# Kernel tuning notes

Measured on AMD Instinct MI355X. Metric: run time of the kernel, lower is better.

## Reference

```python
import jax, jax.numpy as jnp
import numpy as np

B, T, S = 2, 1024, 1024
D, H, L = 512, 8, 4
E, K, FF = 8, 2, 2048
V, BLK = 32000, 2048
DH = D // H
EPS = 1e-5


def setup_inputs() -> dict:
    key = jax.random.key(0)
    ks = jax.random.split(key, 20)
    n = lambda k, shp: jax.random.normal(k, shp, dtype=jnp.float32) * 0.02
    return {
        "decoder_input_ids": jax.random.randint(ks[0], (B, T), 0, V, dtype=jnp.int32),
        "enc_out": jax.random.normal(ks[1], (B, S, D), dtype=jnp.float32),
        "attention_mask": jnp.ones((B, T), dtype=jnp.int32),
        "embed_table": n(ks[2], (V, D)),
        "pos_table": n(ks[3], (BLK, D)),
        "sa_w": n(ks[4], (L, 4, D, D)),   # q,k,v,o projections for self-attn
        "sa_b": jnp.zeros((L, 4, D), jnp.float32),
        "ca_w": n(ks[5], (L, 4, D, D)),   # q,k,v,o projections for cross-attn
        "ca_b": jnp.zeros((L, 4, D), jnp.float32),
        "ln_g": jnp.ones((L, 3, D), jnp.float32),
        "ln_b": jnp.zeros((L, 3, D), jnp.float32),
        "router_w": n(ks[6], (L, D, E)),
        "router_b": jnp.zeros((L, E), jnp.float32),
        "exp_w1": n(ks[7], (L, E, D, FF)),
        "exp_b1": jnp.zeros((L, E, FF), jnp.float32),
        "exp_w2": n(ks[8], (L, E, FF, D)),
        "exp_b2": jnp.zeros((L, E, D), jnp.float32),
    }


def _layer_norm(x, g, b):
    mu = jnp.mean(x, axis=-1, keepdims=True)
    var = jnp.mean(jnp.square(x - mu), axis=-1, keepdims=True)
    return (x - mu) * jax.lax.rsqrt(var + EPS) * g + b


def _mha(q_in, kv_in, w, b, mask):
    # w: [4, D, D]; 0=q,1=k,2=v,3=out
    def split_heads(t):
        Bn, Tn, _ = t.shape
        return t.reshape(Bn, Tn, H, DH).transpose(0, 2, 1, 3)  # [B,H,T,dh]
    q = split_heads(q_in @ w[0] + b[0])
    k = split_heads(kv_in @ w[1] + b[1])
    v = split_heads(kv_in @ w[2] + b[2])
    scores = jnp.einsum("bhqd,bhkd->bhqk", q, k) / jnp.sqrt(jnp.float32(DH))
    if mask is not None:
        scores = jnp.where(mask, scores, jnp.float32(-1e9))
    attn = jax.nn.softmax(scores, axis=-1)
    out = jnp.einsum("bhqk,bhkd->bhqd", attn, v)
    out = out.transpose(0, 2, 1, 3).reshape(q_in.shape[0], q_in.shape[1], D)
    return out @ w[3] + b[3]


def _sparse_moe(x, rw, rb, w1, b1, w2, b2):
    # Router: softmax over experts, keep top-k, renormalize kept weights.
    logits = x @ rw + rb                       # [B,T,E]
    probs = jax.nn.softmax(logits, axis=-1)
    topv, topi = jax.lax.top_k(probs, K)       # [B,T,K]
    kmask = jnp.sum(jax.nn.one_hot(topi, E, dtype=x.dtype), axis=-2)  # [B,T,E]
    gates = probs * kmask
    gates = gates / jnp.sum(gates, axis=-1, keepdims=True)
    # Dense expert compute (faithful math, vectorized over experts).
    h = jax.nn.relu(jnp.einsum("btd,edf->btef", x, w1) + b1)   # [B,T,E,FF]
    eo = jnp.einsum("btef,efd->bted", h, w2) + b2              # [B,T,E,D]
    out = jnp.einsum("bte,bted->btd", gates, eo)
    # Load-balancing aux loss: E * sum_e f_e * P_e
    f = jnp.mean(kmask, axis=(0, 1))
    p = jnp.mean(probs, axis=(0, 1))
    lb = jnp.float32(E) * jnp.sum(f * p)
    return out, lb


def reference(decoder_input_ids, enc_out, attention_mask, embed_table, pos_table,
              sa_w, sa_b, ca_w, ca_b, ln_g, ln_b, router_w, router_b,
              exp_w1, exp_b1, exp_w2, exp_b2):
    Bn, Tn = decoder_input_ids.shape
    y = embed_table[decoder_input_ids] + pos_table[:Tn]  # [B,T,D]
    causal = jnp.tril(jnp.ones((Tn, Tn), dtype=bool))
    am = attention_mask.astype(bool)[:, None, None, :]   # [B,1,1,T]
    mask = causal[None, None] & am                       # [B,1,T,T]
    lb_total = jnp.float32(0.0)
    for i in range(L):
        sa = _mha(y, y, sa_w[i], sa_b[i], mask)
        y = _layer_norm(y + sa, ln_g[i, 0], ln_b[i, 0])
        ca = _mha(y, enc_out, ca_w[i], ca_b[i], None)
        y = _layer_norm(y + ca, ln_g[i, 1], ln_b[i, 1])
        mo, lb = _sparse_moe(y, router_w[i], router_b[i], exp_w1[i], exp_b1[i], exp_w2[i], exp_b2[i])
        lb_total = lb_total + lb
        y = _layer_norm(y + mo, ln_g[i, 2], ln_b[i, 2])
    return y, lb_total
```

## Files before the change

kernel.cpp:

```cpp
#include <hip/hip_runtime.h>
#include <math.h>

#define Bb 2
#define Tt 1024
#define Ss 1024
#define Dd 512
#define Hh 8
#define Ll 4
#define Ee 8
#define FFf 2048
#define Mm 2048
#define NPp 4096
#define EPSF 1e-5f
#define DD_ (Dd*Dd)
#define LOSC 1024.0f
#define ILOSC (1.0f/1024.0f)
#define RBLK 64
#define IMm (1.0f/(float)Mm)

typedef _Float16 f16;
typedef __attribute__((ext_vector_type(8))) _Float16 f16x8;
typedef __attribute__((ext_vector_type(4))) _Float16 f16x4;
typedef __attribute__((ext_vector_type(4))) float f32x4;

__device__ __forceinline__ void fsplit(float x, f16& h, f16& l) {
  h = (f16)x;
  l = (f16)((x - (float)h) * LOSC);
}

__device__ __forceinline__ void load16(const void* g, void* l) {
  __builtin_amdgcn_global_load_lds(
      (const __attribute__((address_space(1))) void*)g,
      (__attribute__((address_space(3))) void*)l, 16, 0, 0);
}

__global__ void embed_kernel(const int* __restrict__ ids,
                             const float* __restrict__ emb,
                             const float* __restrict__ pos,
                             float* __restrict__ Y,
                             f16* __restrict__ Yh, f16* __restrict__ Yl) {
  int m = blockIdx.x;
  int t = m % Tt;
  int id = ids[m];
  for (int d = threadIdx.x; d < Dd; d += 256) {
    float v = emb[(size_t)id * Dd + d] + pos[(size_t)t * Dd + d];
    Y[(size_t)m * Dd + d] = v;
    f16 h, l; fsplit(v, h, l);
    Yh[(size_t)m * Dd + d] = h;
    Yl[(size_t)m * Dd + d] = l;
  }
}

__global__ void cvt_split_kernel(const float* __restrict__ src,
                                 f16* __restrict__ dh, f16* __restrict__ dl) {
  size_t i = ((size_t)blockIdx.x * 256 + threadIdx.x) * 4;
  float4 v = *reinterpret_cast<const float4*>(&src[i]);
  float a[4] = {v.x, v.y, v.z, v.w};
#pragma unroll
  for (int j = 0; j < 4; j++) { f16 h, l; fsplit(a[j], h, l); dh[i + j] = h; dl[i + j] = l; }
}

__global__ __launch_bounds__(256)
void transpose_split(const float* __restrict__ src,
                     f16* __restrict__ dstH, f16* __restrict__ dstL,
                     int Kd, int Nd) {
  __shared__ float Tl[32][33];
  size_t zo = (size_t)blockIdx.z * Kd * Nd;
  int k0 = blockIdx.y * 32, n0 = blockIdx.x * 32;
  int t = threadIdx.x;
  int r = t >> 3, c = t & 7;
  float4 v = *reinterpret_cast<const float4*>(&src[zo + (size_t)(k0 + r) * Nd + n0 + c * 4]);
  Tl[r][c * 4 + 0] = v.x; Tl[r][c * 4 + 1] = v.y;
  Tl[r][c * 4 + 2] = v.z; Tl[r][c * 4 + 3] = v.w;
  __syncthreads();
  int nl = t >> 3, kq = t & 7;
  f16x4 hv, lv;
#pragma unroll
  for (int i = 0; i < 4; i++) {
    f16 h, l; fsplit(Tl[kq * 4 + i][nl], h, l);
    hv[i] = h; lv[i] = l;
  }
  size_t o = zo + (size_t)(n0 + nl) * Kd + k0 + kq * 4;
  *reinterpret_cast<f16x4*>(&dstH[o]) = hv;
  *reinterpret_cast<f16x4*>(&dstL[o]) = lv;
}

template <bool GATHER, bool OSPLIT, bool RELU, bool GATE, int KS>
__global__ __launch_bounds__(256)
void mm128(const f16* __restrict__ Ah_, const f16* __restrict__ Al_, int lda,
           const f16* __restrict__ Bh_, const f16* __restrict__ Bl_,
           const float* __restrict__ bias,
           float* __restrict__ Cf, f16* __restrict__ Ch, f16* __restrict__ Cl, int ldc,
           int Mtot, int N, int K,
           const int* __restrict__ tok, const float* __restrict__ gate,
           const int* __restrict__ offs, const int* __restrict__ cnt) {
  __shared__ f16 Ash[2][128 * 32];
  __shared__ f16 Asl[2][128 * 32];
  __shared__ f16 Bsh[2][128 * 32];
  __shared__ f16 Bsl[2][128 * 32];
  int zz = blockIdx.z;
  int e  = (KS > 1) ? (zz / KS) : zz;
  int ks = (KS > 1) ? (zz % KS) : 0;
  int base = 0, ne = Mtot;
  if (offs) { base = offs[e]; ne = cnt[e]; }
  int m0 = blockIdx.y * 128;
  if (m0 >= ne) return;
  int rem = ne - m0;
  Bh_ += (size_t)e * N * K;
  Bl_ += (size_t)e * N * K;
  bias += (size_t)e * N;
  if (KS > 1) Cf += (size_t)ks * (size_t)Mtot * (size_t)ldc;

  int t = threadIdx.x;
  int rr = t >> 2, cc = t & 3;
  int csw = cc ^ ((rr >> 1) & 3);
  int gr0 = base + m0 + rr;      if (gr0 > Mtot - 1) gr0 = Mtot - 1;
  int gr1 = base + m0 + rr + 64; if (gr1 > Mtot - 1) gr1 = Mtot - 1;
  int arow0 = GATHER ? tok[gr0] : gr0;
  int arow1 = GATHER ? tok[gr1] : gr1;
  size_t aoff0 = (size_t)arow0 * lda + csw * 8;
  size_t aoff1 = (size_t)arow1 * lda + csw * 8;
  size_t boff0 = (size_t)(blockIdx.x * 128 + rr) * K + csw * 8;
  size_t boff1 = (size_t)(blockIdx.x * 128 + rr + 64) * K + csw * 8;

  int lane = t & 63, wv = t >> 6;
  int quad = lane >> 4, m16 = lane & 15;
  int sw = quad ^ ((m16 >> 1) & 3);
  int wm = (wv >> 1) * 64, wn = (wv & 1) * 64;

  f32x4 accm[4][4], accc[4][4];
#pragma unroll
  for (int i = 0; i < 4; i++)
#pragma unroll
    for (int j = 0; j < 4; j++) {
      accm[i][j] = (f32x4){0.f, 0.f, 0.f, 0.f};
      accc[i][j] = (f32x4){0.f, 0.f, 0.f, 0.f};
    }

  int kper = K / KS;
  int kbeg = ks * kper;
  int nt = kper >> 5;

  auto STAGE = [&](int bf, int kc) {
    load16(Ah_ + aoff0 + kc, &Ash[bf][t * 8]);
    load16(Ah_ + aoff1 + kc, &Ash[bf][2048 + t * 8]);
    load16(Al_ + aoff0 + kc, &Asl[bf][t * 8]);
    load16(Al_ + aoff1 + kc, &Asl[bf][2048 + t * 8]);
    load16(Bh_ + boff0 + kc, &Bsh[bf][t * 8]);
    load16(Bh_ + boff1 + kc, &Bsh[bf][2048 + t * 8]);
    load16(Bl_ + boff0 + kc, &Bsl[bf][t * 8]);
    load16(Bl_ + boff1 + kc, &Bsl[bf][2048 + t * 8]);
  };

  STAGE(0, kbeg);
  asm volatile("s_waitcnt vmcnt(0)" ::: "memory");
  __builtin_amdgcn_s_barrier();

  for (int tt = 0; tt < nt; ++tt) {
    int bf = tt & 1;
    if (tt + 1 < nt) STAGE(bf ^ 1, kbeg + (tt + 1) * 32);
    f16x8 ah[4], al[4];
#pragma unroll
    for (int i = 0; i < 4; i++) {
      ah[i] = *reinterpret_cast<const f16x8*>(&Ash[bf][(wm + i * 16 + m16) * 32 + sw * 8]);
      al[i] = *reinterpret_cast<const f16x8*>(&Asl[bf][(wm + i * 16 + m16) * 32 + sw * 8]);
    }
#pragma unroll
    for (int j = 0; j < 4; j++) {
      f16x8 bh = *reinterpret_cast<const f16x8*>(&Bsh[bf][(wn + j * 16 + m16) * 32 + sw * 8]);
      f16x8 bl = *reinterpret_cast<const f16x8*>(&Bsl[bf][(wn + j * 16 + m16) * 32 + sw * 8]);
#pragma unroll
      for (int i = 0; i < 4; i++) {
        accm[i][j] = __builtin_amdgcn_mfma_f32_16x16x32_f16(ah[i], bh, accm[i][j], 0, 0, 0);
        accc[i][j] = __builtin_amdgcn_mfma_f32_16x16x32_f16(ah[i], bl, accc[i][j], 0, 0, 0);
        accc[i][j] = __builtin_amdgcn_mfma_f32_16x16x32_f16(al[i], bh, accc[i][j], 0, 0, 0);
      }
    }
    asm volatile("s_waitcnt vmcnt(0)" ::: "memory");
    __builtin_amdgcn_s_barrier();
  }

#pragma unroll
  for (int i = 0; i < 4; i++) {
#pragma unroll
    for (int reg = 0; reg < 4; reg++) {
      int lr = wm + i * 16 + quad * 4 + reg;
      if (lr < rem) {
        size_t grow = (size_t)(base + m0 + lr);
        float gv = 1.f;
        if (GATE) gv = gate[grow];
#pragma unroll
        for (int j = 0; j < 4; j++) {
          int col = blockIdx.x * 128 + wn + j * 16 + m16;
          float bv = (KS == 1 || ks == 0) ? bias[col] : 0.f;
          float v = accm[i][j][reg] + accc[i][j][reg] * ILOSC + bv;
          if (RELU) v = fmaxf(v, 0.f);
          if (GATE) v *= gv;
          if (OSPLIT) {
            f16 h, l; fsplit(v, h, l);
            Ch[grow * ldc + col] = h;
            Cl[grow * ldc + col] = l;
          } else {
            Cf[grow * ldc + col] = v;
          }
        }
      }
    }
  }
}

__global__ __launch_bounds__(256)
void attn_mfma(const f16* __restrict__ Qh, const f16* __restrict__ Ql, int sq, int oq,
               const f16* __restrict__ Kh, const f16* __restrict__ Kl, int sk, int ok,
               const f16* __restrict__ Vh, const f16* __restrict__ Vl, int sv, int ov,
               f16* __restrict__ Oh, f16* __restrict__ Ol,
               const int* __restrict__ amask, int causal, int nK) {
  __shared__ f16 Ksh[32 * 64];
  __shared__ f16 Ksl[32 * 64];
  __shared__ f16 Vth[64 * 32];
  __shared__ f16 Vtl[64 * 32];
  __shared__ f16 Psh[4 * 16 * 32];
  __shared__ f16 Psl[4 * 16 * 32];

  int bh = blockIdx.x;
  int b = bh >> 3, hd = bh & 7;
  int t = threadIdx.x;
  int wv = t >> 6, lane = t & 63;
  int quad = lane >> 4, m16 = lane & 15;
  int qfrow = blockIdx.y * 64 + wv * 16 + m16;
  int qcbase = blockIdx.y * 64 + wv * 16 + quad * 4;

  size_t qoff = (size_t)(b * Tt + qfrow) * sq + oq + hd * 64;
  f16x8 qh0 = *reinterpret_cast<const f16x8*>(Qh + qoff + quad * 8);
  f16x8 qh1 = *reinterpret_cast<const f16x8*>(Qh + qoff + 32 + quad * 8);
  f16x8 ql0 = *reinterpret_cast<const f16x8*>(Ql + qoff + quad * 8);
  f16x8 ql1 = *reinterpret_cast<const f16x8*>(Ql + qoff + 32 + quad * 8);

  f32x4 Om[4], Oc[4];
#pragma unroll
  for (int c = 0; c < 4; c++) {
    Om[c] = (f32x4){0.f, 0.f, 0.f, 0.f};
    Oc[c] = (f32x4){0.f, 0.f, 0.f, 0.f};
  }
  float mr[4] = {-1e30f, -1e30f, -1e30f, -1e30f};
  float lrw[4] = {0.f, 0.f, 0.f, 0.f};

  int NT = causal ? (blockIdx.y * 2 + 2) : (nK >> 5);
  int myNT = causal ? (((blockIdx.y * 64 + wv * 16 + 15) >> 5) + 1) : NT;

  int rk = t >> 3, gs = t & 7, gsrc = gs ^ (rk & 7);
  int rv = t & 31, gv = t >> 5;

  for (int kt = 0; kt < NT; ++kt) {
    __syncthreads();
    {
      size_t krow = (size_t)(b * 1024 + kt * 32 + rk) * sk + ok + hd * 64 + gsrc * 8;
      *reinterpret_cast<f16x8*>(&Ksh[t * 8]) = *reinterpret_cast<const f16x8*>(Kh + krow);
      *reinterpret_cast<f16x8*>(&Ksl[t * 8]) = *reinterpret_cast<const f16x8*>(Kl + krow);
      size_t vrow = (size_t)(b * 1024 + kt * 32 + rv) * sv + ov + hd * 64 + gv * 8;
      f16x8 vh8 = *reinterpret_cast<const f16x8*>(Vh + vrow);
      f16x8 vl8 = *reinterpret_cast<const f16x8*>(Vl + vrow);
#pragma unroll
      for (int i = 0; i < 8; i++) {
        Vth[(gv * 8 + i) * 32 + rv] = vh8[i];
        Vtl[(gv * 8 + i) * 32 + rv] = vl8[i];
      }
    }
    __syncthreads();

    if (kt < myNT) {
      f32x4 S0m = (f32x4){0.f, 0.f, 0.f, 0.f}, S0c = S0m, S1m = S0m, S1c = S0m;
      {
        int key0 = m16, key1 = 16 + m16;
        int g0a = (quad) ^ (key0 & 7), g0b = (4 + quad) ^ (key0 & 7);
        int g1a = (quad) ^ (key1 & 7), g1b = (4 + quad) ^ (key1 & 7);
        f16x8 kh0a = *reinterpret_cast<const f16x8*>(&Ksh[key0 * 64 + g0a * 8]);
        f16x8 kh0b = *reinterpret_cast<const f16x8*>(&Ksh[key0 * 64 + g0b * 8]);
        f16x8 kl0a = *reinterpret_cast<const f16x8*>(&Ksl[key0 * 64 + g0a * 8]);
        f16x8 kl0b = *reinterpret_cast<const f16x8*>(&Ksl[key0 * 64 + g0b * 8]);
        S0m = __builtin_amdgcn_mfma_f32_16x16x32_f16(qh0, kh0a, S0m, 0, 0, 0);
        S0m = __builtin_amdgcn_mfma_f32_16x16x32_f16(qh1, kh0b, S0m, 0, 0, 0);
        S0c = __builtin_amdgcn_mfma_f32_16x16x32_f16(qh0, kl0a, S0c, 0, 0, 0);
        S0c = __builtin_amdgcn_mfma_f32_16x16x32_f16(qh1, kl0b, S0c, 0, 0, 0);
        S0c = __builtin_amdgcn_mfma_f32_16x16x32_f16(ql0, kh0a, S0c, 0, 0, 0);
        S0c = __builtin_amdgcn_mfma_f32_16x16x32_f16(ql1, kh0b, S0c, 0, 0, 0);
        f16x8 kh1a = *reinterpret_cast<const f16x8*>(&Ksh[key1 * 64 + g1a * 8]);
        f16x8 kh1b = *reinterpret_cast<const f16x8*>(&Ksh[key1 * 64 + g1b * 8]);
        f16x8 kl1a = *reinterpret_cast<const f16x8*>(&Ksl[key1 * 64 + g1a * 8]);
        f16x8 kl1b = *reinterpret_cast<const f16x8*>(&Ksl[key1 * 64 + g1b * 8]);
        S1m = __builtin_amdgcn_mfma_f32_16x16x32_f16(qh0, kh1a, S1m, 0, 0, 0);
        S1m = __builtin_amdgcn_mfma_f32_16x16x32_f16(qh1, kh1b, S1m, 0, 0, 0);
        S1c = __builtin_amdgcn_mfma_f32_16x16x32_f16(qh0, kl1a, S1c, 0, 0, 0);
        S1c = __builtin_amdgcn_mfma_f32_16x16x32_f16(qh1, kl1b, S1c, 0, 0, 0);
        S1c = __builtin_amdgcn_mfma_f32_16x16x32_f16(ql0, kh1a, S1c, 0, 0, 0);
        S1c = __builtin_amdgcn_mfma_f32_16x16x32_f16(ql1, kh1b, S1c, 0, 0, 0);
      }
      float S0[4], S1[4];
      int key0 = kt * 32 + m16, key1 = kt * 32 + 16 + m16;
      int am0 = amask ? amask[b * nK + key0] : 1;
      int am1 = amask ? amask[b * nK + key1] : 1;
#pragma unroll
      for (int reg = 0; reg < 4; reg++) {
        int qr = qcbase + reg;
        bool ok0 = am0 && (!causal || key0 <= qr);
        bool ok1 = am1 && (!causal || key1 <= qr);
        S0[reg] = ok0 ? (S0m[reg] + S0c[reg] * ILOSC) * 0.125f : -1e9f;
        S1[reg] = ok1 ? (S1m[reg] + S1c[reg] * ILOSC) * 0.125f : -1e9f;
      }
      float mt[4], al4[4], rs[4];
#pragma unroll
      for (int reg = 0; reg < 4; reg++) mt[reg] = fmaxf(S0[reg], S1[reg]);
#pragma unroll
      for (int off = 1; off < 16; off <<= 1)
#pragma unroll
        for (int reg = 0; reg < 4; reg++) mt[reg] = fmaxf(mt[reg], __shfl_xor(mt[reg], off, 64));
#pragma unroll
      for (int reg = 0; reg < 4; reg++) {
        float mn = fmaxf(mr[reg], mt[reg]);
        al4[reg] = expf(mr[reg] - mn);
        mr[reg] = mn;
        S0[reg] = expf(S0[reg] - mn);
        S1[reg] = expf(S1[reg] - mn);
        rs[reg] = S0[reg] + S1[reg];
      }
#pragma unroll
      for (int off = 1; off < 16; off <<= 1)
#pragma unroll
        for (int reg = 0; reg < 4; reg++) rs[reg] += __shfl_xor(rs[reg], off, 64);
#pragma unroll
      for (int reg = 0; reg < 4; reg++) {
        lrw[reg] = lrw[reg] * al4[reg] + rs[reg];
#pragma unroll
        for (int c = 0; c < 4; c++) { Om[c][reg] *= al4[reg]; Oc[c][reg] *= al4[reg]; }
        int prow = wv * 16 + quad * 4 + reg;
        f16 ph, pl;
        fsplit(S0[reg], ph, pl);
        Psh[prow * 32 + m16] = ph; Psl[prow * 32 + m16] = pl;
        fsplit(S1[reg], ph, pl);
        Psh[prow * 32 + 16 + m16] = ph; Psl[prow * 32 + 16 + m16] = pl;
      }
      __builtin_amdgcn_sched_barrier(0);
      f16x8 pah = *reinterpret_cast<const f16x8*>(&Psh[(wv * 16 + m16) * 32 + quad * 8]);
      f16x8 pal = *reinterpret_cast<const f16x8*>(&Psl[(wv * 16 + m16) * 32 + quad * 8]);
#pragma unroll
      for (int c = 0; c < 4; c++) {
        f16x8 vbh = *reinterpret_cast<const f16x8*>(&Vth[(c * 16 + m16) * 32 + quad * 8]);
        f16x8 vbl = *reinterpret_cast<const f16x8*>(&Vtl[(c * 16 + m16) * 32 + quad * 8]);
        Om[c] = __builtin_amdgcn_mfma_f32_16x16x32_f16(pah, vbh, Om[c], 0, 0, 0);
        Oc[c] = __builtin_amdgcn_mfma_f32_16x16x32_f16(pah, vbl, Oc[c], 0, 0, 0);
        Oc[c] = __builtin_amdgcn_mfma_f32_16x16x32_f16(pal, vbh, Oc[c], 0, 0, 0);
      }
    }
  }
#pragma unroll
  for (int reg = 0; reg < 4; reg++) {
    int qr = qcbase + reg;
    float inv = 1.f / lrw[reg];
#pragma unroll
    for (int c = 0; c < 4; c++) {
      float o = (Om[c][reg] + Oc[c][reg] * ILOSC) * inv;
      f16 hh, ll; fsplit(o, hh, ll);
      size_t oo = (size_t)(b * Tt + qr) * Dd + hd * 64 + c * 16 + m16;
      Oh[oo] = hh;
      Ol[oo] = ll;
    }
  }
}

__global__ __launch_bounds__(256)
void add_ln_kernel(float* __restrict__ Y, f16* __restrict__ Yh, f16* __restrict__ Yl,
                   const float* __restrict__ Aadd,
                   const float* __restrict__ g, const float* __restrict__ bb) {
  int tid = threadIdx.x;
  size_t base = (size_t)blockIdx.x * Dd;
  __shared__ float red[256];
  __shared__ float mu_s, rs_s;
  float x0 = Y[base + tid] + Aadd[base + tid];
  float x1 = Y[base + 256 + tid] + Aadd[base + 256 + tid];
  red[tid] = x0 + x1; __syncthreads();
  for (int s2 = 128; s2 > 0; s2 >>= 1) { if (tid < s2) red[tid] += red[tid + s2]; __syncthreads(); }
  if (tid == 0) mu_s = red[0] / (float)Dd;
  __syncthreads();
  float mu = mu_s;
  float d0 = x0 - mu, d1 = x1 - mu;
  red[tid] = d0 * d0 + d1 * d1; __syncthreads();
  for (int s2 = 128; s2 > 0; s2 >>= 1) { if (tid < s2) red[tid] += red[tid + s2]; __syncthreads(); }
  if (tid == 0) rs_s = rsqrtf(red[0] / (float)Dd + EPSF);
  __syncthreads();
  float rs = rs_s;
  float o0 = d0 * rs * g[tid] + bb[tid];
  float o1 = d1 * rs * g[256 + tid] + bb[256 + tid];
  f16 h, l;
  Y[base + tid] = o0; fsplit(o0, h, l); Yh[base + tid] = h; Yl[base + tid] = l;
  Y[base + 256 + tid] = o1; fsplit(o1, h, l); Yh[base + 256 + tid] = h; Yl[base + 256 + tid] = l;
}

__global__ __launch_bounds__(256)
void combine_ln_kernel(float* __restrict__ Y, f16* __restrict__ Yh, f16* __restrict__ Yl,
                       const float* __restrict__ pout, const float* __restrict__ pout2,
                       const int* __restrict__ slot,
                       const float* __restrict__ g, const float* __restrict__ bb) {
  int tid = threadIdx.x;
  int m = blockIdx.x;
  size_t base = (size_t)m * Dd;
  int s0 = slot[m * 2 + 0], s1 = slot[m * 2 + 1];
  __shared__ float red[256];
  __shared__ float mu_s, rs_s;
  float x0 = Y[base + tid] + pout[(size_t)s0 * Dd + tid] + pout[(size_t)s1 * Dd + tid]
           + pout2[(size_t)s0 * Dd + tid] + pout2[(size_t)s1 * Dd + tid];
  float x1 = Y[base + 256 + tid] + pout[(size_t)s0 * Dd + 256 + tid] + pout[(size_t)s1 * Dd + 256 + tid]
           + pout2[(size_t)s0 * Dd + 256 + tid] + pout2[(size_t)s1 * Dd + 256 + tid];
  red[tid] = x0 + x1; __syncthreads();
  for (int s2 = 128; s2 > 0; s2 >>= 1) { if (tid < s2) red[tid] += red[tid + s2]; __syncthreads(); }
  if (tid == 0) mu_s = red[0] / (float)Dd;
  __syncthreads();
  float mu = mu_s;
  float d0 = x0 - mu, d1 = x1 - mu;
  red[tid] = d0 * d0 + d1 * d1; __syncthreads();
  for (int s2 = 128; s2 > 0; s2 >>= 1) { if (tid < s2) red[tid] += red[tid + s2]; __syncthreads(); }
  if (tid == 0) rs_s = rsqrtf(red[0] / (float)Dd + EPSF);
  __syncthreads();
  float rs = rs_s;
  float o0 = d0 * rs * g[tid] + bb[tid];
  float o1 = d1 * rs * g[256 + tid] + bb[256 + tid];
  f16 h, l;
  Y[base + tid] = o0; fsplit(o0, h, l); Yh[base + tid] = h; Yl[base + tid] = l;
  Y[base + 256 + tid] = o1; fsplit(o1, h, l); Yh[base + 256 + tid] = h; Yl[base + 256 + tid] = l;
}

__global__ __launch_bounds__(256)
void router_kernel(const float* __restrict__ Y, const float* __restrict__ rw,
                   const float* __restrict__ rb, float* __restrict__ gates,
                   int* __restrict__ topi, int* __restrict__ part_cnt,
                   float* __restrict__ part_sumP) {
  int wv = threadIdx.x >> 6, lane = threadIdx.x & 63;
  __shared__ float wsum[4][Ee];
  __shared__ int wcnt[4][Ee];
  float w[8][Ee];
#pragma unroll
  for (int dd = 0; dd < 8; dd++) {
    const float4* rp = reinterpret_cast<const float4*>(&rw[(size_t)(dd * 64 + lane) * Ee]);
    float4 a = rp[0], b4 = rp[1];
    w[dd][0] = a.x; w[dd][1] = a.y; w[dd][2] = a.z; w[dd][3] = a.w;
    w[dd][4] = b4.x; w[dd][5] = b4.y; w[dd][6] = b4.z; w[dd][7] = b4.w;
  }
  float rbv[Ee];
#pragma unroll
  for (int e = 0; e < Ee; e++) rbv[e] = rb[e];

  float psum[Ee]; int pcnt[Ee];
#pragma unroll
  for (int e = 0; e < Ee; e++) { psum[e] = 0.f; pcnt[e] = 0; }

  int m0 = blockIdx.x * 32 + wv * 8;
  for (int j = 0; j < 8; j++) {
    int m = m0 + j;
    const float* yr = Y + (size_t)m * Dd;
    float yv[8];
#pragma unroll
    for (int dd = 0; dd < 8; dd++) yv[dd] = yr[dd * 64 + lane];
    float acc[Ee];
#pragma unroll
    for (int e = 0; e < Ee; e++) acc[e] = 0.f;
#pragma unroll
    for (int dd = 0; dd < 8; dd++)
#pragma unroll
      for (int e = 0; e < Ee; e++) acc[e] += yv[dd] * w[dd][e];
#pragma unroll
    for (int off = 32; off; off >>= 1)
#pragma unroll
      for (int e = 0; e < Ee; e++) acc[e] += __shfl_xor(acc[e], off, 64);
    if (lane == 0) {
      float pv[Ee];
      float mx = -1e30f;
#pragma unroll
      for (int e = 0; e < Ee; e++) { pv[e] = acc[e] + rbv[e]; mx = fmaxf(mx, pv[e]); }
      float ssum = 0.f;
#pragma unroll
      for (int e = 0; e < Ee; e++) { pv[e] = expf(pv[e] - mx); ssum += pv[e]; }
      float invs = 1.f / ssum;
#pragma unroll
      for (int e = 0; e < Ee; e++) { pv[e] *= invs; psum[e] += pv[e]; }
      int i1 = 0;
#pragma unroll
      for (int e = 1; e < Ee; e++) if (pv[e] > pv[i1]) i1 = e;
      int i2 = (i1 == 0) ? 1 : 0;
#pragma unroll
      for (int e = 0; e < Ee; e++) if (e != i1 && pv[e] > pv[i2]) i2 = e;
      float gs = pv[i1] + pv[i2];
      gates[m * 2 + 0] = pv[i1] / gs;
      gates[m * 2 + 1] = pv[i2] / gs;
      topi[m * 2 + 0] = i1;
      topi[m * 2 + 1] = i2;
#pragma unroll
      for (int e = 0; e < Ee; e++) pcnt[e] += (e == i1) + (e == i2);
    }
  }
  if (lane == 0) {
#pragma unroll
    for (int e = 0; e < Ee; e++) { wsum[wv][e] = psum[e]; wcnt[wv][e] = pcnt[e]; }
  }
  __syncthreads();
  if (threadIdx.x < Ee) {
    int e = threadIdx.x;
    float s = wsum[0][e] + wsum[1][e] + wsum[2][e] + wsum[3][e];
    int c = wcnt[0][e] + wcnt[1][e] + wcnt[2][e] + wcnt[3][e];
    part_sumP[blockIdx.x * Ee + e] = s;
    part_cnt[blockIdx.x * Ee + e] = c;
  }
}

__global__ void prefix_lb_kernel(const int* __restrict__ part_cnt,
                                 const float* __restrict__ part_sumP,
                                 int* __restrict__ cnt, int* __restrict__ offs,
                                 int* __restrict__ fill, float* __restrict__ lb_acc) {
  __shared__ int sc[Ee];
  __shared__ float ss[Ee];
  int t = threadIdx.x;
  if (t < Ee) {
    int c = 0; float s = 0.f;
    for (int b2 = 0; b2 < RBLK; b2++) { c += part_cnt[b2 * Ee + t]; s += part_sumP[b2 * Ee + t]; }
    sc[t] = c; ss[t] = s;
    cnt[t] = c; fill[t] = 0;
  }
  __syncthreads();
  if (t == 0) {
    int run = 0;
    float lb = 0.f;
    for (int e = 0; e < Ee; e++) {
      offs[e] = run; run += sc[e];
      lb += ((float)sc[e] * IMm) * (ss[e] * IMm);
    }
    *lb_acc += (float)Ee * lb;
  }
}

__global__ __launch_bounds__(256)
void scatter_kernel(const int* __restrict__ topi, const float* __restrict__ gates,
                    const int* __restrict__ offs, int* __restrict__ fill,
                    int* __restrict__ pair_tok, float* __restrict__ pair_gate,
                    int* __restrict__ slot) {
  __shared__ int lcnt[Ee];
  __shared__ int lbase[Ee];
  int t = threadIdx.x;
  int m = blockIdx.x * 256 + t;
  if (t < Ee) lcnt[t] = 0;
  __syncthreads();
  int e0 = topi[m * 2 + 0], e1 = topi[m * 2 + 1];
  float g0 = gates[m * 2 + 0], g1 = gates[m * 2 + 1];
  int p0 = atomicAdd(&lcnt[e0], 1);
  int p1 = atomicAdd(&lcnt[e1], 1);
  __syncthreads();
  if (t < Ee) lbase[t] = atomicAdd(&fill[t], lcnt[t]);
  __syncthreads();
  int i0 = offs[e0] + lbase[e0] + p0;
  int i1 = offs[e1] + lbase[e1] + p1;
  pair_tok[i0] = m; pair_gate[i0] = g0; slot[m * 2 + 0] = i0;
  pair_tok[i1] = m; pair_gate[i1] = g1; slot[m * 2 + 1] = i1;
}

__global__ void init_lb_kernel(float* lb_acc) {
  if (threadIdx.x == 0) *lb_acc = 0.f;
}

__global__ void finalize_kernel(const float* __restrict__ Y,
                                const float* __restrict__ lb_acc,
                                float* __restrict__ out) {
  size_t i = (size_t)blockIdx.x * 256 + threadIdx.x;
  const size_t n = (size_t)Mm * Dd;
  if (i < n) out[i] = Y[i];
  if (i == 0) out[n] = *lb_acc;
}

extern "C" void kernel_launch(void* const* d_in, const int* in_sizes, int n_in,
                              void* d_out, int out_size, void* d_ws, size_t ws_size,
                              hipStream_t stream) {
  const int*   ids   = (const int*)d_in[0];
  const float* enc   = (const float*)d_in[1];
  const int*   amask = (const int*)d_in[2];
  const float* emb   = (const float*)d_in[3];
  const float* pos   = (const float*)d_in[4];
  const float* sa_w  = (const float*)d_in[5];
  const float* sa_b  = (const float*)d_in[6];
  const float* ca_w  = (const float*)d_in[7];
  const float* ca_b  = (const float*)d_in[8];
  const float* ln_g  = (const float*)d_in[9];
  const float* ln_b  = (const float*)d_in[10];
  const float* rw    = (const float*)d_in[11];
  const float* rb    = (const float*)d_in[12];
  const float* ew1   = (const float*)d_in[13];
  const float* eb1   = (const float*)d_in[14];
  const float* ew2   = (const float*)d_in[15];
  const float* eb2   = (const float*)d_in[16];
  float* out = (float*)d_out;

  char* p = (char*)d_ws;
  auto alloc = [&](size_t bytes) { void* r = p; p += (bytes + 255) & ~(size_t)255; return r; };
  float* y    = (float*)alloc((size_t)Mm * Dd * 4);
  float* proj = (float*)alloc((size_t)Mm * Dd * 4);
  float* pout = (float*)alloc((size_t)2 * NPp * Dd * 4);
  f16* yh   = (f16*)alloc((size_t)Mm * Dd * 2);
  f16* yl   = (f16*)alloc((size_t)Mm * Dd * 2);
  f16* ench = (f16*)alloc((size_t)Mm * Dd * 2);
  f16* encl = (f16*)alloc((size_t)Mm * Dd * 2);
  f16* qkvh = (f16*)alloc((size_t)Mm * 1536 * 2);
  f16* qkvl = (f16*)alloc((size_t)Mm * 1536 * 2);
  f16* qch  = (f16*)alloc((size_t)Mm * Dd * 2);
  f16* qcl  = (f16*)alloc((size_t)Mm * Dd * 2);
  f16* atth = (f16*)alloc((size_t)Mm * Dd * 2);
  f16* attl = (f16*)alloc((size_t)Mm * Dd * 2);
  f16* ckvh = (f16*)alloc((size_t)Mm * 1024 * 2);
  f16* ckvl = (f16*)alloc((size_t)Mm * 1024 * 2);
  f16* moeh = (f16*)alloc((size_t)NPp * FFf * 2);
  f16* moel = (f16*)alloc((size_t)NPp * FFf * 2);
  f16* saTh = (f16*)alloc((size_t)Ll * 4 * DD_ * 2);
  f16* saTl = (f16*)alloc((size_t)Ll * 4 * DD_ * 2);
  f16* caTh = (f16*)alloc((size_t)Ll * 4 * DD_ * 2);
  f16* caTl = (f16*)alloc((size_t)Ll * 4 * DD_ * 2);
  f16* w1Th = (f16*)alloc((size_t)Ee * Dd * FFf * 2);
  f16* w1Tl = (f16*)alloc((size_t)Ee * Dd * FFf * 2);
  f16* w2Th = (f16*)alloc((size_t)Ee * Dd * FFf * 2);
  f16* w2Tl = (f16*)alloc((size_t)Ee * Dd * FFf * 2);
  float* gates     = (float*)alloc((size_t)Mm * 2 * 4);
  float* pair_gate = (float*)alloc((size_t)NPp * 4);
  float* part_sumP = (float*)alloc((size_t)RBLK * Ee * 4);
  float* lb_acc    = (float*)alloc(4);
  int* topi     = (int*)alloc((size_t)Mm * 2 * 4);
  int* pair_tok = (int*)alloc((size_t)NPp * 4);
  int* slot     = (int*)alloc((size_t)Mm * 2 * 4);
  int* part_cnt = (int*)alloc((size_t)RBLK * Ee * 4);
  int* cnt      = (int*)alloc(Ee * 4);
  int* offs     = (int*)alloc(Ee * 4);
  int* fill     = (int*)alloc(Ee * 4);
  float* pout2 = pout + (size_t)NPp * Dd;

  init_lb_kernel<<<1, 64, 0, stream>>>(lb_acc);
  embed_kernel<<<Mm, 256, 0, stream>>>(ids, emb, pos, y, yh, yl);
  cvt_split_kernel<<<(Mm * Dd) / 1024, 256, 0, stream>>>(enc, ench, encl);
  transpose_split<<<dim3(16, 16, 16), 256, 0, stream>>>(sa_w, saTh, saTl, Dd, Dd);
  transpose_split<<<dim3(16, 16, 16), 256, 0, stream>>>(ca_w, caTh, caTl, Dd, Dd);

  dim3 gAttn(Bb * Hh, Tt / 64);

  for (int i = 0; i < Ll; i++) {
    transpose_split<<<dim3(64, 16, 8), 256, 0, stream>>>(ew1 + (size_t)i * Ee * Dd * FFf, w1Th, w1Tl, Dd, FFf);
    transpose_split<<<dim3(16, 64, 8), 256, 0, stream>>>(ew2 + (size_t)i * Ee * FFf * Dd, w2Th, w2Tl, FFf, Dd);

    const f16* saThl = saTh + (size_t)i * 4 * DD_;
    const f16* saTll = saTl + (size_t)i * 4 * DD_;
    const f16* caThl = caTh + (size_t)i * 4 * DD_;
    const f16* caTll = caTl + (size_t)i * 4 * DD_;
    const float* sabl = sa_b + (size_t)i * 4 * Dd;
    const float* cabl = ca_b + (size_t)i * 4 * Dd;

    mm128<false, true, false, false, 1><<<dim3(8, 16, 1), 256, 0, stream>>>(
        ench, encl, Dd, caThl + DD_, caTll + DD_, cabl + Dd,
        nullptr, ckvh, ckvl, 1024, Mm, 1024, Dd, nullptr, nullptr, nullptr, nullptr);
    mm128<false, true, false, false, 1><<<dim3(12, 16, 1), 256, 0, stream>>>(
        yh, yl, Dd, saThl, saTll, sabl,
        nullptr, qkvh, qkvl, 1536, Mm, 1536, Dd, nullptr, nullptr, nullptr, nullptr);
    attn_mfma<<<gAttn, 256, 0, stream>>>(qkvh, qkvl, 1536, 0, qkvh, qkvl, 1536, 512,
                                         qkvh, qkvl, 1536, 1024, atth, attl, amask, 1, Tt);
    mm128<false, false, false, false, 1><<<dim3(4, 16, 1), 256, 0, stream>>>(
        atth, attl, Dd, saThl + 3 * DD_, saTll + 3 * DD_, sabl + 3 * Dd,
        proj, nullptr, nullptr, Dd, Mm, Dd, Dd, nullptr, nullptr, nullptr, nullptr);
    add_ln_kernel<<<Mm, 256, 0, stream>>>(y, yh, yl, proj,
                                          ln_g + (size_t)(i * 3 + 0) * Dd, ln_b + (size_t)(i * 3 + 0) * Dd);
    mm128<false, true, false, false, 1><<<dim3(4, 16, 1), 256, 0, stream>>>(
        yh, yl, Dd, caThl, caTll, cabl,
        nullptr, qch, qcl, Dd, Mm, Dd, Dd, nullptr, nullptr, nullptr, nullptr);
    attn_mfma<<<gAttn, 256, 0, stream>>>(qch, qcl, Dd, 0, ckvh, ckvl, 1024, 0,
                                         ckvh, ckvl, 1024, 512, atth, attl, nullptr, 0, Ss);
    mm128<false, false, false, false, 1><<<dim3(4, 16, 1), 256, 0, stream>>>(
        atth, attl, Dd, caThl + 3 * DD_, caTll + 3 * DD_, cabl + 3 * Dd,
        proj, nullptr, nullptr, Dd, Mm, Dd, Dd, nullptr, nullptr, nullptr, nullptr);
    add_ln_kernel<<<Mm, 256, 0, stream>>>(y, yh, yl, proj,
                                          ln_g + (size_t)(i * 3 + 1) * Dd, ln_b + (size_t)(i * 3 + 1) * Dd);
    router_kernel<<<RBLK, 256, 0, stream>>>(y, rw + (size_t)i * Dd * Ee, rb + (size_t)i * Ee,
                                            gates, topi, part_cnt, part_sumP);
    prefix_lb_kernel<<<1, 64, 0, stream>>>(part_cnt, part_sumP, cnt, offs, fill, lb_acc);
    scatter_kernel<<<Mm / 256, 256, 0, stream>>>(topi, gates, offs, fill, pair_tok, pair_gate, slot);
    mm128<true, true, true, false, 1><<<dim3(16, 32, 8), 256, 0, stream>>>(
        yh, yl, Dd, w1Th, w1Tl, eb1 + (size_t)i * Ee * FFf,
        nullptr, moeh, moel, FFf, NPp, FFf, Dd, pair_tok, nullptr, offs, cnt);
    mm128<false, false, false, true, 2><<<dim3(4, 32, Ee * 2), 256, 0, stream>>>(
        moeh, moel, FFf, w2Th, w2Tl, eb2 + (size_t)i * Ee * Dd,
        pout, nullptr, nullptr, Dd, NPp, Dd, FFf, nullptr, pair_gate, offs, cnt);
    combine_ln_kernel<<<Mm, 256, 0, stream>>>(y, yh, yl, pout, pout2, slot,
                                              ln_g + (size_t)(i * 3 + 2) * Dd, ln_b + (size_t)(i * 3 + 2) * Dd);
  }

  finalize_kernel<<<(int)(((size_t)Mm * Dd + 256) / 256) + 1, 256, 0, stream>>>(y, lb_acc, out);
}
```

Before: 2.437 ms.

## Pre-tile B weights, interleave MoE hidden hi/lo, and restructure GEMM pipeline waits

New measurement: 2.440 ms. No clear change (+0.1%).

```diff
diff --git a/kernel.cpp b/kernel.cpp
--- a/kernel.cpp
+++ b/kernel.cpp
@@ -80,12 +80,18 @@
     f16 h, l; fsplit(Tl[kq * 4 + i][nl], h, l);
     hv[i] = h; lv[i] = l;
   }
-  size_t o = zo + (size_t)(n0 + nl) * Kd + k0 + kq * 4;
+  int n = n0 + nl;
+  int nb = n >> 7, rr2 = n & 127;
+  int kb = k0 >> 5;
+  int s_orig = kq >> 1;
+  int s_pack = s_orig ^ ((rr2 >> 1) & 3);
+  size_t o = zo + (((size_t)nb * (size_t)(Kd >> 5) + kb) * 128 + rr2) * 32
+           + s_pack * 8 + (kq & 1) * 4;
   *reinterpret_cast<f16x4*>(&dstH[o]) = hv;
   *reinterpret_cast<f16x4*>(&dstL[o]) = lv;
 }
 
-template <bool GATHER, bool OSPLIT, bool RELU, bool GATE, int KS>
+template <bool GATHER, bool OSPLIT, bool RELU, bool GATE, int KS, bool AIL, bool CIL>
 __global__ __launch_bounds__(256)
 void mm128(const f16* __restrict__ Ah_, const f16* __restrict__ Al_, int lda,
            const f16* __restrict__ Bh_, const f16* __restrict__ Bl_,
@@ -118,10 +124,10 @@
   int gr1 = base + m0 + rr + 64; if (gr1 > Mtot - 1) gr1 = Mtot - 1;
   int arow0 = GATHER ? tok[gr0] : gr0;
   int arow1 = GATHER ? tok[gr1] : gr1;
-  size_t aoff0 = (size_t)arow0 * lda + csw * 8;
-  size_t aoff1 = (size_t)arow1 * lda + csw * 8;
-  size_t boff0 = (size_t)(blockIdx.x * 128 + rr) * K + csw * 8;
-  size_t boff1 = (size_t)(blockIdx.x * 128 + rr + 64) * K + csw * 8;
+  const size_t ldaa = (size_t)lda * (AIL ? 2 : 1);
+  size_t aoff0 = (size_t)arow0 * ldaa + csw * 8;
+  size_t aoff1 = (size_t)arow1 * ldaa + csw * 8;
+  size_t btile = (size_t)blockIdx.x * (size_t)(K >> 5) * 4096 + (size_t)t * 8;
 
   int lane = t & 63, wv = t >> 6;
   int quad = lane >> 4, m16 = lane & 15;
@@ -142,23 +148,30 @@
   int nt = kper >> 5;
 
   auto STAGE = [&](int bf, int kc) {
-    load16(Ah_ + aoff0 + kc, &Ash[bf][t * 8]);
-    load16(Ah_ + aoff1 + kc, &Ash[bf][2048 + t * 8]);
-    load16(Al_ + aoff0 + kc, &Asl[bf][t * 8]);
-    load16(Al_ + aoff1 + kc, &Asl[bf][2048 + t * 8]);
-    load16(Bh_ + boff0 + kc, &Bsh[bf][t * 8]);
-    load16(Bh_ + boff1 + kc, &Bsh[bf][2048 + t * 8]);
-    load16(Bl_ + boff0 + kc, &Bsl[bf][t * 8]);
-    load16(Bl_ + boff1 + kc, &Bsl[bf][2048 + t * 8]);
+    int kcA = AIL ? kc * 2 : kc;
+    load16(Ah_ + aoff0 + kcA, &Ash[bf][t * 8]);
+    load16(Ah_ + aoff1 + kcA, &Ash[bf][2048 + t * 8]);
+    load16(Al_ + aoff0 + kcA, &Asl[bf][t * 8]);
+    load16(Al_ + aoff1 + kcA, &Asl[bf][2048 + t * 8]);
+    size_t bb = btile + (size_t)(kc >> 5) * 4096;
+    load16(Bh_ + bb, &Bsh[bf][t * 8]);
+    load16(Bh_ + bb + 2048, &Bsh[bf][2048 + t * 8]);
+    load16(Bl_ + bb, &Bsl[bf][t * 8]);
+    load16(Bl_ + bb + 2048, &Bsl[bf][2048 + t * 8]);
   };
 
+  asm volatile("s_waitcnt vmcnt(0)" ::: "memory");
   STAGE(0, kbeg);
-  asm volatile("s_waitcnt vmcnt(0)" ::: "memory");
-  __builtin_amdgcn_s_barrier();
 
   for (int tt = 0; tt < nt; ++tt) {
     int bf = tt & 1;
-    if (tt + 1 < nt) STAGE(bf ^ 1, kbeg + (tt + 1) * 32);
+    if (tt + 1 < nt) {
+      STAGE(bf ^ 1, kbeg + (tt + 1) * 32);
+      asm volatile("s_waitcnt vmcnt(8)" ::: "memory");
+    } else {
+      asm volatile("s_waitcnt vmcnt(0)" ::: "memory");
+    }
+    __builtin_amdgcn_s_barrier();
     f16x8 ah[4], al[4];
 #pragma unroll
     for (int i = 0; i < 4; i++) {
@@ -176,7 +189,6 @@
         accc[i][j] = __builtin_amdgcn_mfma_f32_16x16x32_f16(al[i], bh, accc[i][j], 0, 0, 0);
       }
     }
-    asm volatile("s_waitcnt vmcnt(0)" ::: "memory");
     __builtin_amdgcn_s_barrier();
   }
 
@@ -198,8 +210,14 @@
           if (GATE) v *= gv;
           if (OSPLIT) {
             f16 h, l; fsplit(v, h, l);
-            Ch[grow * ldc + col] = h;
-            Cl[grow * ldc + col] = l;
+            if (CIL) {
+              size_t idx = grow * ((size_t)ldc * 2) + (size_t)((col >> 5) * 64 + (col & 31));
+              Ch[idx] = h;
+              Cl[idx] = l;
+            } else {
+              Ch[grow * ldc + col] = h;
+              Cl[grow * ldc + col] = l;
+            }
           } else {
             Cf[grow * ldc + col] = v;
           }
@@ -611,8 +629,7 @@
   f16* attl = (f16*)alloc((size_t)Mm * Dd * 2);
   f16* ckvh = (f16*)alloc((size_t)Mm * 1024 * 2);
   f16* ckvl = (f16*)alloc((size_t)Mm * 1024 * 2);
-  f16* moeh = (f16*)alloc((size_t)NPp * FFf * 2);
-  f16* moel = (f16*)alloc((size_t)NPp * FFf * 2);
+  f16* moe  = (f16*)alloc((size_t)NPp * FFf * 2 * 2);
   f16* saTh = (f16*)alloc((size_t)Ll * 4 * DD_ * 2);
   f16* saTl = (f16*)alloc((size_t)Ll * 4 * DD_ * 2);
   f16* caTh = (f16*)alloc((size_t)Ll * 4 * DD_ * 2);
@@ -653,25 +670,25 @@
     const float* sabl = sa_b + (size_t)i * 4 * Dd;
     const float* cabl = ca_b + (size_t)i * 4 * Dd;
 
-    mm128<false, true, false, false, 1><<<dim3(8, 16, 1), 256, 0, stream>>>(
+    mm128<false, true, false, false, 1, false, false><<<dim3(8, 16, 1), 256, 0, stream>>>(
         ench, encl, Dd, caThl + DD_, caTll + DD_, cabl + Dd,
         nullptr, ckvh, ckvl, 1024, Mm, 1024, Dd, nullptr, nullptr, nullptr, nullptr);
-    mm128<false, true, false, false, 1><<<dim3(12, 16, 1), 256, 0, stream>>>(
+    mm128<false, true, false, false, 1, false, false><<<dim3(12, 16, 1), 256, 0, stream>>>(
         yh, yl, Dd, saThl, saTll, sabl,
         nullptr, qkvh, qkvl, 1536, Mm, 1536, Dd, nullptr, nullptr, nullptr, nullptr);
     attn_mfma<<<gAttn, 256, 0, stream>>>(qkvh, qkvl, 1536, 0, qkvh, qkvl, 1536, 512,
                                          qkvh, qkvl, 1536, 1024, atth, attl, amask, 1, Tt);
-    mm128<false, false, false, false, 1><<<dim3(4, 16, 1), 256, 0, stream>>>(
+    mm128<false, false, false, false, 1, false, false><<<dim3(4, 16, 1), 256, 0, stream>>>(
         atth, attl, Dd, saThl + 3 * DD_, saTll + 3 * DD_, sabl + 3 * Dd,
         proj, nullptr, nullptr, Dd, Mm, Dd, Dd, nullptr, nullptr, nullptr, nullptr);
     add_ln_kernel<<<Mm, 256, 0, stream>>>(y, yh, yl, proj,
                                           ln_g + (size_t)(i * 3 + 0) * Dd, ln_b + (size_t)(i * 3 + 0) * Dd);
-    mm128<false, true, false, false, 1><<<dim3(4, 16, 1), 256, 0, stream>>>(
+    mm128<false, true, false, false, 1, false, false><<<dim3(4, 16, 1), 256, 0, stream>>>(
         yh, yl, Dd, caThl, caTll, cabl,
         nullptr, qch, qcl, Dd, Mm, Dd, Dd, nullptr, nullptr, nullptr, nullptr);
     attn_mfma<<<gAttn, 256, 0, stream>>>(qch, qcl, Dd, 0, ckvh, ckvl, 1024, 0,
                                          ckvh, ckvl, 1024, 512, atth, attl, nullptr, 0, Ss);
-    mm128<false, false, false, false, 1><<<dim3(4, 16, 1), 256, 0, stream>>>(
+    mm128<false, false, false, false, 1, false, false><<<dim3(4, 16, 1), 256, 0, stream>>>(
         atth, attl, Dd, caThl + 3 * DD_, caTll + 3 * DD_, cabl + 3 * Dd,
         proj, nullptr, nullptr, Dd, Mm, Dd, Dd, nullptr, nullptr, nullptr, nullptr);
     add_ln_kernel<<<Mm, 256, 0, stream>>>(y, yh, yl, proj,
@@ -680,11 +697,11 @@
                                             gates, topi, part_cnt, part_sumP);
     prefix_lb_kernel<<<1, 64, 0, stream>>>(part_cnt, part_sumP, cnt, offs, fill, lb_acc);
     scatter_kernel<<<Mm / 256, 256, 0, stream>>>(topi, gates, offs, fill, pair_tok, pair_gate, slot);
-    mm128<true, true, true, false, 1><<<dim3(16, 32, 8), 256, 0, stream>>>(
+    mm128<true, true, true, false, 1, false, true><<<dim3(16, 32, 8), 256, 0, stream>>>(
         yh, yl, Dd, w1Th, w1Tl, eb1 + (size_t)i * Ee * FFf,
-        nullptr, moeh, moel, FFf, NPp, FFf, Dd, pair_tok, nullptr, offs, cnt);
-    mm128<false, false, false, true, 2><<<dim3(4, 32, Ee * 2), 256, 0, stream>>>(
-        moeh, moel, FFf, w2Th, w2Tl, eb2 + (size_t)i * Ee * Dd,
+        nullptr, moe, moe + 32, FFf, NPp, FFf, Dd, pair_tok, nullptr, offs, cnt);
+    mm128<false, false, false, true, 2, true, false><<<dim3(4, 32, Ee * 2), 256, 0, stream>>>(
+        moe, moe + 32, FFf, w2Th, w2Tl, eb2 + (size_t)i * Ee * Dd,
         pout, nullptr, nullptr, Dd, NPp, Dd, FFf, nullptr, pair_gate, offs, cnt);
     combine_ln_kernel<<<Mm, 256, 0, stream>>>(y, yh, yl, pout, pout2, slot,
                                               ln_g + (size_t)(i * 3 + 2) * Dd, ln_b + (size_t)(i * 3 + 2) * Dd);
```
